# Performance work log

Measured on AMD Instinct MI355X. Metric: run time of the kernel, lower is better.

The kernel has to match this reference:

```python
import jax, jax.numpy as jnp
import numpy as np


def setup_inputs() -> dict:
    key = jax.random.key(0)
    x = jax.random.normal(key, (8192, 1024), dtype=jnp.float32)
    return {"x": x}


def reference(x):
    # attn_scores = x @ x.T  -> [N, N]
    scores = jnp.einsum('nd,md->nm', x, x)
    # softmax over last dim (stable)
    weights = jax.nn.softmax(scores, axis=-1)
    # context = weights @ x -> [N, d]
    return jnp.einsum('nm,md->nd', weights, x)
```

## Files before the change

### kernel.cpp

```cpp
#include <hip/hip_runtime.h>
#include <hip/hip_bf16.h>
#include <cstdint>

#define NROWS 8192
#define DDIM  1024
#define QBLK  32
#define KVT   256
#define NW    8
#define NITER (NROWS / KVT)
#define KS_S  (DDIM / 32)
#define KS_PV (KVT / 32)
#define LOG2E 1.44269504088896340736f

typedef __attribute__((ext_vector_type(4))) float f32x4;
typedef __attribute__((ext_vector_type(8))) short bf16x8;
typedef unsigned short u16;

__device__ __forceinline__ u16 f2bf(float f) {
  uint32_t u = __builtin_bit_cast(uint32_t, f);
  uint32_t r = u + 0x7FFFu + ((u >> 16) & 1u);
  return (u16)(r >> 16);
}
__device__ __forceinline__ bf16x8 asbf(int4 v) { return __builtin_bit_cast(bf16x8, v); }

__global__ __launch_bounds__(256) void prep_kernel(const float* __restrict__ x,
                                                   u16* __restrict__ xbf,
                                                   u16* __restrict__ xbfT) {
  __shared__ __align__(16) u16 T[64][72];
  const int t = threadIdx.x;
  const int n0 = blockIdx.x * 64;
  const int d0 = blockIdx.y * 64;
#pragma unroll
  for (int rr = 0; rr < 4; ++rr) {
    const int row = (t >> 4) + rr * 16;
    const int c4 = (t & 15) * 4;
    const float4 v = *reinterpret_cast<const float4*>(&x[(size_t)(n0 + row) * DDIM + d0 + c4]);
    ushort4 b;
    b.x = f2bf(v.x); b.y = f2bf(v.y); b.z = f2bf(v.z); b.w = f2bf(v.w);
    *reinterpret_cast<ushort4*>(&xbf[(size_t)(n0 + row) * DDIM + d0 + c4]) = b;
    *reinterpret_cast<ushort4*>(&T[row][c4]) = b;
  }
  __syncthreads();
#pragma unroll
  for (int rr = 0; rr < 4; ++rr) {
    const int drow = (t >> 4) + rr * 16;
    const int nc = (t & 15) * 4;
    ushort4 o;
    o.x = T[nc + 0][drow]; o.y = T[nc + 1][drow];
    o.z = T[nc + 2][drow]; o.w = T[nc + 3][drow];
    *reinterpret_cast<ushort4*>(&xbfT[(size_t)(d0 + drow) * NROWS + n0 + nc]) = o;
  }
}

__global__ __launch_bounds__(512, 2) void attn_kernel(const u16* __restrict__ xbf,
                                                      const u16* __restrict__ xbfT,
                                                      float* __restrict__ out) {
  __shared__ __align__(16) u16 Qf[QBLK][DDIM + 8];
  __shared__ __align__(16) u16 Ps[QBLK][KVT + 8];
  __shared__ float smax[NW][QBLK];
  __shared__ float ssum[NW][QBLK];

  const int tid = threadIdx.x;
  const int w = tid >> 6;
  const int lane = tid & 63;
  const int g = lane >> 4;
  const int ln16 = lane & 15;
  const int j = lane & 31;
  const int q0 = blockIdx.x * QBLK;

  {
    const int qr = tid >> 4;
    const int qc0 = (tid & 15) * 64;
#pragma unroll
    for (int i = 0; i < 8; ++i) {
      const int4 v = *reinterpret_cast<const int4*>(&xbf[(size_t)(q0 + qr) * DDIM + qc0 + i * 8]);
      *reinterpret_cast<int4*>(&Qf[qr][qc0 + i * 8]) = v;
    }
  }
  __syncthreads();

  f32x4 oacc[2][8];
#pragma unroll
  for (int qf = 0; qf < 2; ++qf)
#pragma unroll
    for (int c = 0; c < 8; ++c) oacc[qf][c] = (f32x4){0.f, 0.f, 0.f, 0.f};
  float m_run = -INFINITY, l_run = 0.0f;

  for (int t = 0; t < NITER; ++t) {
    const int kvb = t * KVT;

    const u16* kbase = xbf + (size_t)(kvb + w * 32) * DDIM + g * 8;
    f32x4 sacc[2][2] = {{{0.f,0.f,0.f,0.f},{0.f,0.f,0.f,0.f}},
                        {{0.f,0.f,0.f,0.f},{0.f,0.f,0.f,0.f}}};
    int4 kb[4][2];
#pragma unroll
    for (int p = 0; p < 3; ++p) {
      kb[p][0] = *reinterpret_cast<const int4*>(kbase + (size_t)ln16 * DDIM + p * 32);
      kb[p][1] = *reinterpret_cast<const int4*>(kbase + (size_t)(16 + ln16) * DDIM + p * 32);
    }
#pragma unroll
    for (int ks = 0; ks < KS_S; ++ks) {
      if (ks + 3 < KS_S) {
        kb[(ks + 3) & 3][0] = *reinterpret_cast<const int4*>(kbase + (size_t)ln16 * DDIM + (ks + 3) * 32);
        kb[(ks + 3) & 3][1] = *reinterpret_cast<const int4*>(kbase + (size_t)(16 + ln16) * DDIM + (ks + 3) * 32);
      }
      const bf16x8 a0 = *reinterpret_cast<const bf16x8*>(&Qf[ln16][ks * 32 + g * 8]);
      const bf16x8 a1 = *reinterpret_cast<const bf16x8*>(&Qf[16 + ln16][ks * 32 + g * 8]);
      const bf16x8 b0 = asbf(kb[ks & 3][0]);
      const bf16x8 b1 = asbf(kb[ks & 3][1]);
      sacc[0][0] = __builtin_amdgcn_mfma_f32_16x16x32_bf16(a0, b0, sacc[0][0], 0, 0, 0);
      sacc[1][0] = __builtin_amdgcn_mfma_f32_16x16x32_bf16(a1, b0, sacc[1][0], 0, 0, 0);
      sacc[0][1] = __builtin_amdgcn_mfma_f32_16x16x32_bf16(a0, b1, sacc[0][1], 0, 0, 0);
      sacc[1][1] = __builtin_amdgcn_mfma_f32_16x16x32_bf16(a1, b1, sacc[1][1], 0, 0, 0);
    }

    float rmx[2][4];
#pragma unroll
    for (int qf = 0; qf < 2; ++qf)
#pragma unroll
      for (int r = 0; r < 4; ++r) {
        float v = fmaxf(sacc[qf][0][r], sacc[qf][1][r]);
        v = fmaxf(v, __shfl_xor(v, 1, 16));
        v = fmaxf(v, __shfl_xor(v, 2, 16));
        v = fmaxf(v, __shfl_xor(v, 4, 16));
        v = fmaxf(v, __shfl_xor(v, 8, 16));
        rmx[qf][r] = v;
      }
    if (ln16 == 0) {
#pragma unroll
      for (int qf = 0; qf < 2; ++qf)
#pragma unroll
        for (int r = 0; r < 4; ++r) smax[w][qf * 16 + g * 4 + r] = rmx[qf][r];
    }
    __syncthreads();
    float tm = smax[0][j];
#pragma unroll
    for (int wv = 1; wv < NW; ++wv) tm = fmaxf(tm, smax[wv][j]);
    const float mnew = fmaxf(m_run, tm);
    const float alpha = exp2f((m_run - mnew) * LOG2E);
    m_run = mnew;

    float mrow[2][4], arow[2][4];
#pragma unroll
    for (int qf = 0; qf < 2; ++qf)
#pragma unroll
      for (int r = 0; r < 4; ++r) {
        mrow[qf][r] = __shfl(mnew, qf * 16 + g * 4 + r);
        arow[qf][r] = __shfl(alpha, qf * 16 + g * 4 + r);
      }

    float rs[2][4];
#pragma unroll
    for (int qf = 0; qf < 2; ++qf)
#pragma unroll
      for (int r = 0; r < 4; ++r) {
        const float p0 = exp2f((sacc[qf][0][r] - mrow[qf][r]) * LOG2E);
        const float p1 = exp2f((sacc[qf][1][r] - mrow[qf][r]) * LOG2E);
        Ps[qf * 16 + g * 4 + r][w * 32 + ln16]      = f2bf(p0);
        Ps[qf * 16 + g * 4 + r][w * 32 + 16 + ln16] = f2bf(p1);
        float s = p0 + p1;
        s += __shfl_xor(s, 1, 16);
        s += __shfl_xor(s, 2, 16);
        s += __shfl_xor(s, 4, 16);
        s += __shfl_xor(s, 8, 16);
        rs[qf][r] = s;
      }
    if (ln16 == 0) {
#pragma unroll
      for (int qf = 0; qf < 2; ++qf)
#pragma unroll
        for (int r = 0; r < 4; ++r) ssum[w][qf * 16 + g * 4 + r] = rs[qf][r];
    }
    __syncthreads();
    float ts = ssum[0][j];
#pragma unroll
    for (int wv = 1; wv < NW; ++wv) ts += ssum[wv][j];
    l_run = l_run * alpha + ts;

#pragma unroll
    for (int qf = 0; qf < 2; ++qf)
#pragma unroll
      for (int cf = 0; cf < 8; ++cf)
#pragma unroll
        for (int r = 0; r < 4; ++r) oacc[qf][cf][r] *= arow[qf][r];

    const u16* vbase = xbfT + (size_t)(w * 128 + ln16) * NROWS + kvb + g * 8;
    int4 vv[2][8];
#pragma unroll
    for (int cf = 0; cf < 8; ++cf)
      vv[0][cf] = *reinterpret_cast<const int4*>(vbase + (size_t)(cf * 16) * NROWS);
#pragma unroll
    for (int ks = 0; ks < KS_PV; ++ks) {
      const int cur = ks & 1;
      if (ks + 1 < KS_PV) {
#pragma unroll
        for (int cf = 0; cf < 8; ++cf)
          vv[cur ^ 1][cf] = *reinterpret_cast<const int4*>(
              vbase + (size_t)(cf * 16) * NROWS + (ks + 1) * 32);
      }
      const bf16x8 pa0 = *reinterpret_cast<const bf16x8*>(&Ps[ln16][ks * 32 + g * 8]);
      const bf16x8 pa1 = *reinterpret_cast<const bf16x8*>(&Ps[16 + ln16][ks * 32 + g * 8]);
      __builtin_amdgcn_s_setprio(1);
#pragma unroll
      for (int cf = 0; cf < 8; ++cf) {
        oacc[0][cf] = __builtin_amdgcn_mfma_f32_16x16x32_bf16(pa0, asbf(vv[cur][cf]), oacc[0][cf], 0, 0, 0);
        oacc[1][cf] = __builtin_amdgcn_mfma_f32_16x16x32_bf16(pa1, asbf(vv[cur][cf]), oacc[1][cf], 0, 0, 0);
      }
      __builtin_amdgcn_s_setprio(0);
    }
  }

  const float rinv = 1.0f / l_run;
  float rrow[2][4];
#pragma unroll
  for (int qf = 0; qf < 2; ++qf)
#pragma unroll
    for (int r = 0; r < 4; ++r) rrow[qf][r] = __shfl(rinv, qf * 4 == 0 ? g * 4 + r : qf * 16 + g * 4 + r);
#pragma unroll
  for (int qf = 0; qf < 2; ++qf)
#pragma unroll
    for (int cf = 0; cf < 8; ++cf)
#pragma unroll
      for (int r = 0; r < 4; ++r) {
        const int row = q0 + qf * 16 + g * 4 + r;
        const int c = w * 128 + cf * 16 + ln16;
        out[(size_t)row * DDIM + c] = oacc[qf][cf][r] * rrow[qf][r];
      }
}

extern "C" void kernel_launch(void* const* d_in, const int* in_sizes, int n_in,
                              void* d_out, int out_size, void* d_ws, size_t ws_size,
                              hipStream_t stream) {
  const float* x = (const float*)d_in[0];
  u16* xbf  = (u16*)d_ws;
  u16* xbfT = xbf + (size_t)NROWS * DDIM;
  float* out = (float*)d_out;

  hipLaunchKernelGGL(prep_kernel, dim3(NROWS / 64, DDIM / 64), dim3(256), 0, stream,
                     x, xbf, xbfT);
  hipLaunchKernelGGL(attn_kernel, dim3(NROWS / QBLK), dim3(512), 0, stream,
                     xbf, xbfT, out);
}
```

Before: 1.060 ms.

## Prefetch next K tile during PV phase with explicit vmcnt-managed loads

Global loads of K and V now go through inline-asm dwordx4 loads, with explicit s_waitcnt vmcnt counts and scheduling barriers, so each MFMA step waits only for the buffer it consumes. The first three K slices of the next KV tile are issued before the PV stage, which hides their latency behind the V loads and the PV MFMAs instead of stalling at the start of the next iteration. The hand-tuned wait counts must match the exact load issue order, and opaque asm loads take scheduling freedom away from the compiler. A redundant shuffle-index expression is also simplified.

```diff
diff --git a/kernel.cpp b/kernel.cpp
--- a/kernel.cpp
+++ b/kernel.cpp
@@ -16,6 +16,17 @@
 typedef __attribute__((ext_vector_type(8))) short bf16x8;
 typedef unsigned short u16;
 
+__device__ __forceinline__ int4 gload16(const u16* p) {
+  int4 r;
+  asm volatile("global_load_dwordx4 %0, %1, off" : "=v"(r) : "v"(p));
+  return r;
+}
+#define VM_WAIT(N)                                     \
+  do {                                                 \
+    asm volatile("s_waitcnt vmcnt(" #N ")" ::: "memory"); \
+    __builtin_amdgcn_sched_barrier(0);                 \
+  } while (0)
+
 __device__ __forceinline__ u16 f2bf(float f) {
   uint32_t u = __builtin_bit_cast(uint32_t, f);
   uint32_t r = u + 0x7FFFu + ((u >> 16) & 1u);
@@ -86,26 +97,32 @@
     for (int c = 0; c < 8; ++c) oacc[qf][c] = (f32x4){0.f, 0.f, 0.f, 0.f};
   float m_run = -INFINITY, l_run = 0.0f;
 
+  const u16* kp0 = xbf + (size_t)(w * 32 + ln16) * DDIM + g * 8;
+  const u16* kp1 = xbf + (size_t)(w * 32 + 16 + ln16) * DDIM + g * 8;
+  int4 kb[4][2];
+#pragma unroll
+  for (int p = 0; p < 3; ++p) {
+    kb[p][0] = gload16(kp0 + p * 32);
+    kb[p][1] = gload16(kp1 + p * 32);
+  }
+
   for (int t = 0; t < NITER; ++t) {
     const int kvb = t * KVT;
 
-    const u16* kbase = xbf + (size_t)(kvb + w * 32) * DDIM + g * 8;
     f32x4 sacc[2][2] = {{{0.f,0.f,0.f,0.f},{0.f,0.f,0.f,0.f}},
                         {{0.f,0.f,0.f,0.f},{0.f,0.f,0.f,0.f}}};
-    int4 kb[4][2];
-#pragma unroll
-    for (int p = 0; p < 3; ++p) {
-      kb[p][0] = *reinterpret_cast<const int4*>(kbase + (size_t)ln16 * DDIM + p * 32);
-      kb[p][1] = *reinterpret_cast<const int4*>(kbase + (size_t)(16 + ln16) * DDIM + p * 32);
-    }
 #pragma unroll
     for (int ks = 0; ks < KS_S; ++ks) {
       if (ks + 3 < KS_S) {
-        kb[(ks + 3) & 3][0] = *reinterpret_cast<const int4*>(kbase + (size_t)ln16 * DDIM + (ks + 3) * 32);
-        kb[(ks + 3) & 3][1] = *reinterpret_cast<const int4*>(kbase + (size_t)(16 + ln16) * DDIM + (ks + 3) * 32);
+        kb[(ks + 3) & 3][0] = gload16(kp0 + (ks + 3) * 32);
+        kb[(ks + 3) & 3][1] = gload16(kp1 + (ks + 3) * 32);
       }
       const bf16x8 a0 = *reinterpret_cast<const bf16x8*>(&Qf[ln16][ks * 32 + g * 8]);
       const bf16x8 a1 = *reinterpret_cast<const bf16x8*>(&Qf[16 + ln16][ks * 32 + g * 8]);
+      if (ks < KS_S - 3)       VM_WAIT(6);
+      else if (ks == KS_S - 3) VM_WAIT(4);
+      else if (ks == KS_S - 2) VM_WAIT(2);
+      else                     VM_WAIT(0);
       const bf16x8 b0 = asbf(kb[ks & 3][0]);
       const bf16x8 b1 = asbf(kb[ks & 3][1]);
       sacc[0][0] = __builtin_amdgcn_mfma_f32_16x16x32_bf16(a0, b0, sacc[0][0], 0, 0, 0);
@@ -184,22 +201,33 @@
 #pragma unroll
         for (int r = 0; r < 4; ++r) oacc[qf][cf][r] *= arow[qf][r];
 
-    const u16* vbase = xbfT + (size_t)(w * 128 + ln16) * NROWS + kvb + g * 8;
+    if (t + 1 < NITER) {
+      kp0 += (size_t)KVT * DDIM;
+      kp1 += (size_t)KVT * DDIM;
+#pragma unroll
+      for (int p = 0; p < 3; ++p) {
+        kb[p][0] = gload16(kp0 + p * 32);
+        kb[p][1] = gload16(kp1 + p * 32);
+      }
+    }
+
+    const u16* vb = xbfT + (size_t)(w * 128 + ln16) * NROWS + kvb + g * 8;
     int4 vv[2][8];
 #pragma unroll
     for (int cf = 0; cf < 8; ++cf)
-      vv[0][cf] = *reinterpret_cast<const int4*>(vbase + (size_t)(cf * 16) * NROWS);
+      vv[0][cf] = gload16(vb + (size_t)(cf * 16) * NROWS);
 #pragma unroll
     for (int ks = 0; ks < KS_PV; ++ks) {
       const int cur = ks & 1;
       if (ks + 1 < KS_PV) {
 #pragma unroll
         for (int cf = 0; cf < 8; ++cf)
-          vv[cur ^ 1][cf] = *reinterpret_cast<const int4*>(
-              vbase + (size_t)(cf * 16) * NROWS + (ks + 1) * 32);
+          vv[cur ^ 1][cf] = gload16(vb + (size_t)(cf * 16) * NROWS + (ks + 1) * 32);
       }
       const bf16x8 pa0 = *reinterpret_cast<const bf16x8*>(&Ps[ln16][ks * 32 + g * 8]);
       const bf16x8 pa1 = *reinterpret_cast<const bf16x8*>(&Ps[16 + ln16][ks * 32 + g * 8]);
+      if (ks < KS_PV - 1) VM_WAIT(8);
+      else                VM_WAIT(0);
       __builtin_amdgcn_s_setprio(1);
 #pragma unroll
       for (int cf = 0; cf < 8; ++cf) {
@@ -215,7 +243,7 @@
 #pragma unroll
   for (int qf = 0; qf < 2; ++qf)
 #pragma unroll
-    for (int r = 0; r < 4; ++r) rrow[qf][r] = __shfl(rinv, qf * 4 == 0 ? g * 4 + r : qf * 16 + g * 4 + r);
+    for (int r = 0; r < 4; ++r) rrow[qf][r] = __shfl(rinv, qf * 16 + g * 4 + r);
 #pragma unroll
   for (int qf = 0; qf < 2; ++qf)
 #pragma unroll
```

Measured after the change: 1.059 ms. Within noise of the previous version (-0.0%).
